# Kernel tuning notes

Hardware: AMD Instinct MI355X
Metric: run time of the kernel (lower is better)

## Reference

```python
import jax, jax.numpy as jnp
import numpy as np

M1 = M2 = M3 = 8  # retained modes per spatial dim


def get_3d_clifford_kernel(w, g):
    # w: (8, O, I, 2m1, 2m2, 2m3); returns (8O, 8I, 2m1, 2m2, 2m3)
    g0, g1, g2 = g[0], g[1], g[2]
    k0 = jnp.concatenate([w[0], w[1] * g0, w[2] * g1, w[3] * g2, -w[4] * g0 * g1, -w[5] * g0 * g2, -w[6] * g1 * g2, -w[7] * g0 * g1 * g2], axis=1)
    k1 = jnp.concatenate([w[1], w[0], -w[4] * g1, -w[5] * g2, w[2] * g1, w[3] * g2, -w[7] * g1 * g2, -w[6] * g1 * g2], axis=1)
    k2 = jnp.concatenate([w[2], w[4] * g0, w[0], -w[6] * g2, -w[1] * g0, w[7] * g0 * g2, w[3] * g2, w[5] * g0 * g2], axis=1)
    k3 = jnp.concatenate([w[3], w[5] * g0, w[6] * g1, w[0], -w[7] * g0 * g1, -w[1] * g0, -w[2] * g1, -w[4] * g0 * g1], axis=1)
    k4 = jnp.concatenate([w[4], w[2], -w[1], g2 * w[7], w[0], -w[6] * g2, w[5] * g2, w[3] * g2], axis=1)
    k5 = jnp.concatenate([w[5], w[3], -w[7] * g1, -w[1], w[6] * g1, w[0], -w[4] * g1, -w[2] * g1], axis=1)
    k6 = jnp.concatenate([w[6], w[7] * g0, w[3], -w[2], -w[5] * g0, w[4] * g0, w[0], w[1] * g0], axis=1)
    k7 = jnp.concatenate([w[7], w[6], -w[5], w[4], w[3], -w[2], w[1], w[0]], axis=1)
    return jnp.concatenate([k0, k1, k2, k3, k4, k5, k6, k7], axis=0)


def setup_inputs() -> dict:
    key = jax.random.key(0)
    k1, k2 = jax.random.split(key)
    B, D, H, W, Cin, Cout = 4, 48, 48, 48, 24, 24
    x = jax.random.normal(k1, (B, D, H, W, Cin, 8), dtype=jnp.float32)
    scale = 1.0 / (Cin * Cout)
    weights = scale * jax.random.uniform(k2, (8, Cout, Cin, 2 * M1, 2 * M2, 2 * M3), dtype=jnp.float32)
    return {"x": x, "weights": weights}


def reference(x, weights):
    B, D, H, W, Cin, _ = x.shape
    Cout = weights.shape[1]
    g = jnp.ones(3, dtype=x.dtype)  # metric (1, 1, 1)
    # complex-dual packing of the 8 blades
    d1 = x[..., 0] + 1j * x[..., 7]
    d2 = x[..., 1] + 1j * x[..., 6]
    d3 = x[..., 2] + 1j * x[..., 5]
    d4 = x[..., 3] + 1j * x[..., 4]
    f1 = jnp.fft.fftn(d1, axes=(1, 2, 3))
    f2 = jnp.fft.fftn(d2, axes=(1, 2, 3))
    f3 = jnp.fft.fftn(d3, axes=(1, 2, 3))
    f4 = jnp.fft.fftn(d4, axes=(1, 2, 3))
    bchw = lambda t: t.transpose(0, 4, 1, 2, 3)
    # (B, 8*Cin, D, H, W) real tensor of blade spectra
    mv_ft = jnp.concatenate([bchw(f1.real), bchw(f2.real), bchw(f3.real), bchw(f4.real),
                             bchw(f4.imag), bchw(f3.imag), bchw(f2.imag), bchw(f1.imag)], axis=1)
    # gather the 8 low/high-frequency octant corners -> (B, 8Cin, 2m1, 2m2, 2m3)
    i1 = jnp.concatenate([jnp.arange(M1), jnp.arange(D - M1, D)])
    i2 = jnp.concatenate([jnp.arange(M2), jnp.arange(H - M2, H)])
    i3 = jnp.concatenate([jnp.arange(M3), jnp.arange(W - M3, W)])
    input_mul = mv_ft[:, :, i1[:, None, None], i2[None, :, None], i3[None, None, :]]
    kernel = get_3d_clifford_kernel(weights, g)  # (8Cout, 8Cin, 2m1, 2m2, 2m3)
    output_mul = jnp.einsum("bixyz,oixyz->boxyz", input_mul, kernel)
    # scatter back to full spectrum
    out_ft = jnp.zeros((B, 8 * Cout, D, H, W), dtype=mv_ft.dtype)
    out_ft = out_ft.at[:, :, i1[:, None, None], i2[None, :, None], i3[None, None, :]].set(output_mul)
    out_ft = out_ft.reshape(B, 8, Cout, D, H, W).transpose(0, 2, 3, 4, 5, 1)  # (B, Cout, D, H, W, 8)
    o1 = out_ft[..., 0] + 1j * out_ft[..., 7]
    o2 = out_ft[..., 1] + 1j * out_ft[..., 6]
    o3 = out_ft[..., 2] + 1j * out_ft[..., 5]
    o4 = out_ft[..., 3] + 1j * out_ft[..., 4]
    g1_ = jnp.fft.ifftn(o1, axes=(2, 3, 4))
    g2_ = jnp.fft.ifftn(o2, axes=(2, 3, 4))
    g3_ = jnp.fft.ifftn(o3, axes=(2, 3, 4))
    g4_ = jnp.fft.ifftn(o4, axes=(2, 3, 4))
    output = jnp.stack([g1_.real, g2_.real, g3_.real, g4_.real,
                        g4_.imag, g3_.imag, g2_.imag, g1_.imag], axis=-1)  # (B, Cout, D, H, W, 8)
    return output.transpose(0, 2, 3, 4, 1, 5)  # (B, D, H, W, Cout, 8)
```

## Files before the change

kernel.cpp:

```cpp
#include <hip/hip_runtime.h>
#include <math.h>


#define C866 0.8660254037844386f

constexpr float FC0[8] = {1.0f, 0.99144486137885f, 0.96592582628907f, 0.92387953251129f,
                          0.86602540378444f, 0.79335334029124f, 0.70710678118655f, 0.60876142900872f};
constexpr float FS0[8] = {0.0f, 0.13052619222005f, 0.25881904510252f, 0.38268343236509f,
                          0.5f, 0.60876142900872f, 0.70710678118655f, 0.79335334029124f};
constexpr float FC1[8] = {0.5f, 0.60876142900872f, 0.70710678118655f, 0.79335334029124f,
                          0.86602540378444f, 0.92387953251129f, 0.96592582628907f, 0.99144486137885f};
constexpr float FS1[8] = {-0.86602540378444f, -0.79335334029124f, -0.70710678118655f, -0.60876142900872f,
                          -0.5f, -0.38268343236509f, -0.25881904510252f, -0.13052619222005f};

__device__ __forceinline__ float2 cmul(float2 a, float2 b) {
  return make_float2(fmaf(a.x, b.x, -(a.y * b.y)), fmaf(a.x, b.y, a.y * b.x));
}
__device__ __forceinline__ void cfma(float2& acc, float2 a, float2 t) {
  acc.x = fmaf(a.x, t.x, acc.x); acc.x = fmaf(-a.y, t.y, acc.x);
  acc.y = fmaf(a.x, t.y, acc.y); acc.y = fmaf(a.y, t.x, acc.y);
}

struct FwdState {
  float2 acc[8], t[8], stp[8];
  float2 R1, R2;
};

__device__ __forceinline__ void fwd_init(FwdState& st, int half) {
#pragma unroll
  for (int r = 0; r < 8; ++r) {
    st.acc[r] = make_float2(0.f, 0.f);
    st.t[r] = make_float2(1.f, 0.f);
    st.stp[r] = make_float2(half ? FC1[r] : FC0[r],
                            half ? -FS1[r] : -FS0[r]);
  }
  st.R1 = half ? make_float2(-0.5f, -C866) : make_float2(1.f, 0.f);
  st.R2 = half ? make_float2(-0.5f,  C866) : make_float2(1.f, 0.f);
}

__device__ __forceinline__ void fwd_stepf(FwdState& st, float2 z0, float2 z1, float2 z2) {
  z1 = cmul(z1, st.R1);
  z2 = cmul(z2, st.R2);
  const float sx = z1.x + z2.x, sy = z1.y + z2.y;
  const float dx = z1.x - z2.x, dy = z1.y - z2.y;
  const float2 y0 = make_float2(z0.x + sx, z0.y + sy);
  const float tx = fmaf(-0.5f, sx, z0.x), ty = fmaf(-0.5f, sy, z0.y);
  const float ex = C866 * dx, ey = C866 * dy;
  const float2 y1 = make_float2(tx + ey, ty - ex);
  const float2 y2 = make_float2(tx - ey, ty + ex);
#pragma unroll
  for (int r = 0; r < 8; ++r) {
    const float2 yy = (r % 3 == 0) ? y0 : ((r % 3 == 1) ? y1 : y2);
    cfma(st.acc[r], yy, st.t[r]);
    st.t[r] = cmul(st.t[r], st.stp[r]);
  }
}

struct InvState {
  float2 zr[16], t[16];
};

__device__ __forceinline__ void inv_init(InvState& st) {
#pragma unroll
  for (int m = 0; m < 16; ++m) st.t[m] = make_float2(1.f, 0.f);
}

__device__ __forceinline__ void inv_stepf(InvState& st, float2& o0, float2& o1, float2& o2) {
  constexpr int JG[16] = {0,1,2,0,1,2,0,1, 1,2,0,1,2,0,1,2};
  float2 u0 = make_float2(0.f, 0.f), u1 = u0, u2 = u0;
#pragma unroll
  for (int m = 0; m < 16; ++m) {
    float2& uu = (JG[m] == 0) ? u0 : ((JG[m] == 1) ? u1 : u2);
    cfma(uu, st.zr[m], st.t[m]);
    const float2 stp = (m < 8) ? make_float2(FC0[m], FS0[m])
                               : make_float2(FC1[m - 8], FS1[m - 8]);
    st.t[m] = cmul(st.t[m], stp);
  }
  const float sx = u1.x + u2.x, sy = u1.y + u2.y;
  const float dx = u1.x - u2.x, dy = u1.y - u2.y;
  o0 = make_float2(u0.x + sx, u0.y + sy);
  const float tx = fmaf(-0.5f, sx, u0.x), ty = fmaf(-0.5f, sy, u0.y);
  const float ex = C866 * dx, ey = C866 * dy;
  o1 = make_float2(tx - ey, ty + ex);
  o2 = make_float2(tx + ey, ty - ex);
}

__global__ __launch_bounds__(192) void k_fwd_w(const float* __restrict__ x,
                                               float2* __restrict__ A) {
  __shared__ __align__(16) float2 xs[48 * 96];
  {
    const float* xp = x + (size_t)blockIdx.x * 9216;
    for (int idx = threadIdx.x; idx < 1152; idx += 192) {
      const int w = idx / 24, ci = idx % 24;
      const float4 u = *(const float4*)(xp + w * 192 + ci * 8);
      const float4 v = *(const float4*)(xp + w * 192 + ci * 8 + 4);
      float4* dst = (float4*)(&xs[w * 96 + ci * 4]);
      dst[0] = make_float4(u.x, v.w, u.y, v.z);
      dst[1] = make_float4(u.z, v.y, u.w, v.x);
    }
  }
  __syncthreads();

  const int q = threadIdx.x % 96, half = threadIdx.x / 96;
  FwdState st;
  fwd_init(st, half);
#pragma unroll 4
  for (int j = 0; j < 16; ++j) {
    const float2 z0 = xs[j * 96 + q];
    const float2 z1 = xs[(j + 16) * 96 + q];
    const float2 z2 = xs[(j + 32) * 96 + q];
    fwd_stepf(st, z0, z1, z2);
  }
  float2* Ap = A + (size_t)blockIdx.x * 1536 + q;
#pragma unroll
  for (int r = 0; r < 8; ++r) Ap[(half * 8 + r) * 96] = st.acc[r];
}

__global__ __launch_bounds__(192) void k_fwd_h(const float2* __restrict__ A,
                                               float2* __restrict__ Bv) {
  const int k3 = blockIdx.x & 15, bd = blockIdx.x >> 4;
  const int q = threadIdx.x % 96, half = threadIdx.x / 96;
  const float2* Ap = A + ((size_t)bd * 768 + k3) * 96 + q;
  FwdState st;
  fwd_init(st, half);
  for (int j = 0; j < 16; ++j) {
    const float2 z0 = Ap[(size_t)j * 1536];
    const float2 z1 = Ap[(size_t)(j + 16) * 1536];
    const float2 z2 = Ap[(size_t)(j + 32) * 1536];
    fwd_stepf(st, z0, z1, z2);
  }
  float2* Bp = Bv + ((size_t)bd * 256 + k3) * 96 + q;
#pragma unroll
  for (int r = 0; r < 8; ++r) Bp[(size_t)(half * 8 + r) * 1536] = st.acc[r];
}

__global__ __launch_bounds__(192) void k_fwd_d(const float2* __restrict__ Bv,
                                               float2* __restrict__ Cv) {
  const int k23 = blockIdx.x & 255, b = blockIdx.x >> 8;
  const int q = threadIdx.x % 96, half = threadIdx.x / 96;
  const float2* Bp = Bv + ((size_t)b * 12288 + k23) * 96 + q;
  FwdState st;
  fwd_init(st, half);
  for (int j = 0; j < 16; ++j) {
    const float2 z0 = Bp[(size_t)j * 24576];
    const float2 z1 = Bp[(size_t)(j + 16) * 24576];
    const float2 z2 = Bp[(size_t)(j + 32) * 24576];
    fwd_stepf(st, z0, z1, z2);
  }
  float2* Cp = Cv + ((size_t)b * 4096 + k23) * 96 + q;
#pragma unroll
  for (int r = 0; r < 8; ++r) Cp[(size_t)(half * 8 + r) * 24576] = st.acc[r];
}

__global__ __launch_bounds__(256) void k_einsum(const float2* __restrict__ Cv,
                                                const float* __restrict__ wgt,
                                                float2* __restrict__ OMz) {
  const int mode = blockIdx.x * 64 + (threadIdx.x & 63);
  const int co = blockIdx.y * 4 + (threadIdx.x >> 6);

  constexpr int WIDX[8][8] = {
      {0, 1, 2, 3, 4, 5, 6, 7}, {1, 0, 4, 5, 2, 3, 7, 6},
      {2, 4, 0, 6, 1, 7, 3, 5}, {3, 5, 6, 0, 7, 1, 2, 4},
      {4, 2, 1, 7, 0, 6, 5, 3}, {5, 3, 7, 1, 6, 0, 4, 2},
      {6, 7, 3, 2, 5, 4, 0, 1}, {7, 6, 5, 4, 3, 2, 1, 0}};
  constexpr int SGN[8][8] = {
      {1, 1, 1, 1, -1, -1, -1, -1}, {1, 1, -1, -1, 1, 1, -1, -1},
      {1, 1, 1, -1, -1, 1, 1, 1},   {1, 1, 1, 1, -1, -1, -1, -1},
      {1, 1, -1, 1, 1, -1, 1, 1},   {1, 1, -1, -1, 1, 1, -1, -1},
      {1, 1, 1, -1, -1, 1, 1, 1},   {1, 1, -1, 1, 1, -1, 1, 1}};

  float acc[8][4];
#pragma unroll
  for (int bo = 0; bo < 8; ++bo)
#pragma unroll
    for (int b = 0; b < 4; ++b) acc[bo][b] = 0.f;

  for (int ci = 0; ci < 24; ++ci) {
    float w8[8];
#pragma unroll
    for (int k = 0; k < 8; ++k)
      w8[k] = wgt[(size_t)((k * 24 + co) * 24 + ci) * 4096 + mode];
#pragma unroll
    for (int b = 0; b < 4; ++b) {
      const float4* cp =
          (const float4*)(Cv + ((size_t)(b * 4096 + mode) * 96 + ci * 4));
      const float4 u = cp[0], v = cp[1];
      const float inv[8] = {u.x, u.z, v.x, v.z, v.w, v.y, u.w, u.y};
#pragma unroll
      for (int bo = 0; bo < 8; ++bo) {
#pragma unroll
        for (int bi = 0; bi < 8; ++bi) {
          const float wv = w8[WIDX[bo][bi]];
          if (SGN[bo][bi] > 0)
            acc[bo][b] = fmaf(wv, inv[bi], acc[bo][b]);
          else
            acc[bo][b] = fmaf(wv, -inv[bi], acc[bo][b]);
        }
      }
    }
  }
#pragma unroll
  for (int b = 0; b < 4; ++b) {
    float2* op = OMz + ((size_t)(b * 4096 + mode) * 96 + co * 4);
#pragma unroll
    for (int c = 0; c < 4; ++c) op[c] = make_float2(acc[c][b], acc[7 - c][b]);
  }
}

__global__ __launch_bounds__(192) void k_inv_d(const float2* __restrict__ OMz,
                                               float2* __restrict__ IS1) {
  const int col = blockIdx.x * 2 + threadIdx.x / 96;
  const int q = threadIdx.x % 96;
  const int k23 = col & 255, b = col >> 8;
  InvState st;
#pragma unroll
  for (int m = 0; m < 16; ++m)
    st.zr[m] = OMz[((size_t)b * 4096 + m * 256 + k23) * 96 + q];
  inv_init(st);
  float2* Op = IS1 + ((size_t)b * 12288 + k23) * 96 + q;
  for (int j = 0; j < 16; ++j) {
    float2 o0, o1, o2;
    inv_stepf(st, o0, o1, o2);
    Op[(size_t)j * 24576] = o0;
    Op[(size_t)(j + 16) * 24576] = o1;
    Op[(size_t)(j + 32) * 24576] = o2;
  }
}

__global__ __launch_bounds__(192) void k_inv_h(const float2* __restrict__ IS1,
                                               float2* __restrict__ IS2) {
  const int col = blockIdx.x * 2 + threadIdx.x / 96;
  const int q = threadIdx.x % 96;
  const int m3 = col & 15, bd = col >> 4;
  InvState st;
#pragma unroll
  for (int m = 0; m < 16; ++m)
    st.zr[m] = IS1[((size_t)bd * 256 + m * 16 + m3) * 96 + q];
  inv_init(st);
  float2* Op = IS2 + ((size_t)bd * 768 + m3) * 96 + q;
  for (int j = 0; j < 16; ++j) {
    float2 o0, o1, o2;
    inv_stepf(st, o0, o1, o2);
    Op[(size_t)j * 1536] = o0;
    Op[(size_t)(j + 16) * 1536] = o1;
    Op[(size_t)(j + 32) * 1536] = o2;
  }
}

__global__ __launch_bounds__(192) void k_inv_w(const float2* __restrict__ IS2,
                                               float* __restrict__ out) {
  const int blk = blockIdx.x * 2 + threadIdx.x / 96;
  const int q = threadIdx.x % 96;
  const int co = q >> 2, c = q & 3;
  const float norm = 1.0f / 110592.0f;
  InvState st;
#pragma unroll
  for (int m = 0; m < 16; ++m) {
    float2 z = IS2[((size_t)blk * 16 + m) * 96 + q];
    st.zr[m] = make_float2(z.x * norm, z.y * norm);
  }
  inv_init(st);
  float* ob = out + (size_t)blk * 9216 + co * 8;
  for (int j = 0; j < 16; ++j) {
    float2 o0, o1, o2;
    inv_stepf(st, o0, o1, o2);
    float* p0 = ob + (size_t)j * 192;
    float* p1 = ob + (size_t)(j + 16) * 192;
    float* p2 = ob + (size_t)(j + 32) * 192;
    p0[c] = o0.x; p0[7 - c] = o0.y;
    p1[c] = o1.x; p1[7 - c] = o1.y;
    p2[c] = o2.x; p2[7 - c] = o2.y;
  }
}

extern "C" void kernel_launch(void* const* d_in, const int* in_sizes, int n_in,
                              void* d_out, int out_size, void* d_ws, size_t ws_size,
                              hipStream_t stream) {
  (void)in_sizes; (void)n_in; (void)out_size; (void)ws_size;
  const float* x = (const float*)d_in[0];
  const float* wgt = (const float*)d_in[1];
  float* out = (float*)d_out;

  char* ob = (char*)d_out;
  float2* A   = (float2*)(ob + 0);
  float2* Bv  = (float2*)(ob + 113246208);
  float2* Cv  = (float2*)(ob + 150994944);
  float2* OMz = (float2*)(ob + 163577856);
  float2* IS1 = (float2*)(ob + 0);
  float2* IS2 = (float2*)d_ws;

  k_fwd_w<<<9216, 192, 0, stream>>>(x, A);
  k_fwd_h<<<3072, 192, 0, stream>>>(A, Bv);
  k_fwd_d<<<1024, 192, 0, stream>>>(Bv, Cv);
  k_einsum<<<dim3(64, 6), 256, 0, stream>>>(Cv, wgt, OMz);
  k_inv_d<<<512, 192, 0, stream>>>(OMz, IS1);
  k_inv_h<<<1536, 192, 0, stream>>>(IS1, IS2);
  k_inv_w<<<4608, 192, 0, stream>>>(IS2, out);
}
```

Baseline: 351.2 us.

## Store FFT intermediates as fp16 and split einsum reduction over Cin halves

Intermediate spectra between the FFT stages (and the input staged in shared memory) are now stored as packed half-precision complex pairs instead of float2. This halves the global and shared memory traffic of these bandwidth-bound passes. Separately, the einsum kernel doubles its block size and splits the Cin loop across two thread groups, combining their partial sums through shared memory to get more parallelism. The fp16 storage reduces accuracy and risks overflow or precision loss against the fp32 reference.

```diff
diff --git a/kernel.cpp b/kernel.cpp
--- a/kernel.cpp
+++ b/kernel.cpp
@@ -12,6 +12,17 @@
                           0.86602540378444f, 0.92387953251129f, 0.96592582628907f, 0.99144486137885f};
 constexpr float FS1[8] = {-0.86602540378444f, -0.79335334029124f, -0.70710678118655f, -0.60876142900872f,
                           -0.5f, -0.38268343236509f, -0.25881904510252f, -0.13052619222005f};
+
+__device__ __forceinline__ uint32_t c2h(float2 z) {
+  union { _Float16 h[2]; uint32_t u; } v;
+  v.h[0] = (_Float16)z.x; v.h[1] = (_Float16)z.y;
+  return v.u;
+}
+__device__ __forceinline__ float2 h2c(uint32_t u) {
+  union { uint32_t u; _Float16 h[2]; } v;
+  v.u = u;
+  return make_float2((float)v.h[0], (float)v.h[1]);
+}
 
 __device__ __forceinline__ float2 cmul(float2 a, float2 b) {
   return make_float2(fmaf(a.x, b.x, -(a.y * b.y)), fmaf(a.x, b.y, a.y * b.x));
@@ -86,17 +97,20 @@
 }
 
 __global__ __launch_bounds__(192) void k_fwd_w(const float* __restrict__ x,
-                                               float2* __restrict__ A) {
-  __shared__ __align__(16) float2 xs[48 * 96];
+                                               uint32_t* __restrict__ A) {
+  __shared__ __align__(16) uint32_t xs[48 * 96];
   {
     const float* xp = x + (size_t)blockIdx.x * 9216;
     for (int idx = threadIdx.x; idx < 1152; idx += 192) {
       const int w = idx / 24, ci = idx % 24;
       const float4 u = *(const float4*)(xp + w * 192 + ci * 8);
       const float4 v = *(const float4*)(xp + w * 192 + ci * 8 + 4);
-      float4* dst = (float4*)(&xs[w * 96 + ci * 4]);
-      dst[0] = make_float4(u.x, v.w, u.y, v.z);
-      dst[1] = make_float4(u.z, v.y, u.w, v.x);
+      uint4 d;
+      d.x = c2h(make_float2(u.x, v.w));
+      d.y = c2h(make_float2(u.y, v.z));
+      d.z = c2h(make_float2(u.z, v.y));
+      d.w = c2h(make_float2(u.w, v.x));
+      *(uint4*)(&xs[w * 96 + ci * 4]) = d;
     }
   }
   __syncthreads();
@@ -106,45 +120,45 @@
   fwd_init(st, half);
 #pragma unroll 4
   for (int j = 0; j < 16; ++j) {
-    const float2 z0 = xs[j * 96 + q];
-    const float2 z1 = xs[(j + 16) * 96 + q];
-    const float2 z2 = xs[(j + 32) * 96 + q];
+    const float2 z0 = h2c(xs[j * 96 + q]);
+    const float2 z1 = h2c(xs[(j + 16) * 96 + q]);
+    const float2 z2 = h2c(xs[(j + 32) * 96 + q]);
     fwd_stepf(st, z0, z1, z2);
   }
-  float2* Ap = A + (size_t)blockIdx.x * 1536 + q;
-#pragma unroll
-  for (int r = 0; r < 8; ++r) Ap[(half * 8 + r) * 96] = st.acc[r];
-}
-
-__global__ __launch_bounds__(192) void k_fwd_h(const float2* __restrict__ A,
-                                               float2* __restrict__ Bv) {
+  uint32_t* Ap = A + (size_t)blockIdx.x * 1536 + q;
+#pragma unroll
+  for (int r = 0; r < 8; ++r) Ap[(half * 8 + r) * 96] = c2h(st.acc[r]);
+}
+
+__global__ __launch_bounds__(192) void k_fwd_h(const uint32_t* __restrict__ A,
+                                               uint32_t* __restrict__ Bv) {
   const int k3 = blockIdx.x & 15, bd = blockIdx.x >> 4;
   const int q = threadIdx.x % 96, half = threadIdx.x / 96;
-  const float2* Ap = A + ((size_t)bd * 768 + k3) * 96 + q;
+  const uint32_t* Ap = A + ((size_t)bd * 768 + k3) * 96 + q;
   FwdState st;
   fwd_init(st, half);
   for (int j = 0; j < 16; ++j) {
-    const float2 z0 = Ap[(size_t)j * 1536];
-    const float2 z1 = Ap[(size_t)(j + 16) * 1536];
-    const float2 z2 = Ap[(size_t)(j + 32) * 1536];
+    const float2 z0 = h2c(Ap[(size_t)j * 1536]);
+    const float2 z1 = h2c(Ap[(size_t)(j + 16) * 1536]);
+    const float2 z2 = h2c(Ap[(size_t)(j + 32) * 1536]);
     fwd_stepf(st, z0, z1, z2);
   }
-  float2* Bp = Bv + ((size_t)bd * 256 + k3) * 96 + q;
-#pragma unroll
-  for (int r = 0; r < 8; ++r) Bp[(size_t)(half * 8 + r) * 1536] = st.acc[r];
-}
-
-__global__ __launch_bounds__(192) void k_fwd_d(const float2* __restrict__ Bv,
+  uint32_t* Bp = Bv + ((size_t)bd * 256 + k3) * 96 + q;
+#pragma unroll
+  for (int r = 0; r < 8; ++r) Bp[(size_t)(half * 8 + r) * 1536] = c2h(st.acc[r]);
+}
+
+__global__ __launch_bounds__(192) void k_fwd_d(const uint32_t* __restrict__ Bv,
                                                float2* __restrict__ Cv) {
   const int k23 = blockIdx.x & 255, b = blockIdx.x >> 8;
   const int q = threadIdx.x % 96, half = threadIdx.x / 96;
-  const float2* Bp = Bv + ((size_t)b * 12288 + k23) * 96 + q;
+  const uint32_t* Bp = Bv + ((size_t)b * 12288 + k23) * 96 + q;
   FwdState st;
   fwd_init(st, half);
   for (int j = 0; j < 16; ++j) {
-    const float2 z0 = Bp[(size_t)j * 24576];
-    const float2 z1 = Bp[(size_t)(j + 16) * 24576];
-    const float2 z2 = Bp[(size_t)(j + 32) * 24576];
+    const float2 z0 = h2c(Bp[(size_t)j * 24576]);
+    const float2 z1 = h2c(Bp[(size_t)(j + 16) * 24576]);
+    const float2 z2 = h2c(Bp[(size_t)(j + 32) * 24576]);
     fwd_stepf(st, z0, z1, z2);
   }
   float2* Cp = Cv + ((size_t)b * 4096 + k23) * 96 + q;
@@ -152,11 +166,16 @@
   for (int r = 0; r < 8; ++r) Cp[(size_t)(half * 8 + r) * 24576] = st.acc[r];
 }
 
-__global__ __launch_bounds__(256) void k_einsum(const float2* __restrict__ Cv,
+__global__ __launch_bounds__(512) void k_einsum(const float2* __restrict__ Cv,
                                                 const float* __restrict__ wgt,
                                                 float2* __restrict__ OMz) {
-  const int mode = blockIdx.x * 64 + (threadIdx.x & 63);
-  const int co = blockIdx.y * 4 + (threadIdx.x >> 6);
+  const int lane = threadIdx.x & 63;
+  const int mode = blockIdx.x * 64 + lane;
+  const int sub = threadIdx.x >> 6;
+  const int col = sub & 3;
+  const int cih = sub >> 2;
+  const int co = blockIdx.y * 4 + col;
+  const int ci0 = cih * 12;
 
   constexpr int WIDX[8][8] = {
       {0, 1, 2, 3, 4, 5, 6, 7}, {1, 0, 4, 5, 2, 3, 7, 6},
@@ -175,7 +194,7 @@
 #pragma unroll
     for (int b = 0; b < 4; ++b) acc[bo][b] = 0.f;
 
-  for (int ci = 0; ci < 24; ++ci) {
+  for (int ci = ci0; ci < ci0 + 12; ++ci) {
     float w8[8];
 #pragma unroll
     for (int k = 0; k < 8; ++k)
@@ -199,16 +218,31 @@
       }
     }
   }
-#pragma unroll
-  for (int b = 0; b < 4; ++b) {
-    float2* op = OMz + ((size_t)(b * 4096 + mode) * 96 + co * 4);
-#pragma unroll
-    for (int c = 0; c < 4; ++c) op[c] = make_float2(acc[c][b], acc[7 - c][b]);
+
+  __shared__ float red[32][4][64];
+  if (cih == 1) {
+#pragma unroll
+    for (int bo = 0; bo < 8; ++bo)
+#pragma unroll
+      for (int b = 0; b < 4; ++b) red[bo * 4 + b][col][lane] = acc[bo][b];
+  }
+  __syncthreads();
+  if (cih == 0) {
+#pragma unroll
+    for (int bo = 0; bo < 8; ++bo)
+#pragma unroll
+      for (int b = 0; b < 4; ++b) acc[bo][b] += red[bo * 4 + b][col][lane];
+#pragma unroll
+    for (int b = 0; b < 4; ++b) {
+      float2* op = OMz + ((size_t)(b * 4096 + mode) * 96 + co * 4);
+#pragma unroll
+      for (int c = 0; c < 4; ++c) op[c] = make_float2(acc[c][b], acc[7 - c][b]);
+    }
   }
 }
 
 __global__ __launch_bounds__(192) void k_inv_d(const float2* __restrict__ OMz,
-                                               float2* __restrict__ IS1) {
+                                               uint32_t* __restrict__ IS1) {
   const int col = blockIdx.x * 2 + threadIdx.x / 96;
   const int q = threadIdx.x % 96;
   const int k23 = col & 255, b = col >> 8;
@@ -217,37 +251,37 @@
   for (int m = 0; m < 16; ++m)
     st.zr[m] = OMz[((size_t)b * 4096 + m * 256 + k23) * 96 + q];
   inv_init(st);
-  float2* Op = IS1 + ((size_t)b * 12288 + k23) * 96 + q;
+  uint32_t* Op = IS1 + ((size_t)b * 12288 + k23) * 96 + q;
   for (int j = 0; j < 16; ++j) {
     float2 o0, o1, o2;
     inv_stepf(st, o0, o1, o2);
-    Op[(size_t)j * 24576] = o0;
-    Op[(size_t)(j + 16) * 24576] = o1;
-    Op[(size_t)(j + 32) * 24576] = o2;
-  }
-}
-
-__global__ __launch_bounds__(192) void k_inv_h(const float2* __restrict__ IS1,
-                                               float2* __restrict__ IS2) {
+    Op[(size_t)j * 24576] = c2h(o0);
+    Op[(size_t)(j + 16) * 24576] = c2h(o1);
+    Op[(size_t)(j + 32) * 24576] = c2h(o2);
+  }
+}
+
+__global__ __launch_bounds__(192) void k_inv_h(const uint32_t* __restrict__ IS1,
+                                               uint32_t* __restrict__ IS2) {
   const int col = blockIdx.x * 2 + threadIdx.x / 96;
   const int q = threadIdx.x % 96;
   const int m3 = col & 15, bd = col >> 4;
   InvState st;
 #pragma unroll
   for (int m = 0; m < 16; ++m)
-    st.zr[m] = IS1[((size_t)bd * 256 + m * 16 + m3) * 96 + q];
+    st.zr[m] = h2c(IS1[((size_t)bd * 256 + m * 16 + m3) * 96 + q]);
   inv_init(st);
-  float2* Op = IS2 + ((size_t)bd * 768 + m3) * 96 + q;
+  uint32_t* Op = IS2 + ((size_t)bd * 768 + m3) * 96 + q;
   for (int j = 0; j < 16; ++j) {
     float2 o0, o1, o2;
     inv_stepf(st, o0, o1, o2);
-    Op[(size_t)j * 1536] = o0;
-    Op[(size_t)(j + 16) * 1536] = o1;
-    Op[(size_t)(j + 32) * 1536] = o2;
-  }
-}
-
-__global__ __launch_bounds__(192) void k_inv_w(const float2* __restrict__ IS2,
+    Op[(size_t)j * 1536] = c2h(o0);
+    Op[(size_t)(j + 16) * 1536] = c2h(o1);
+    Op[(size_t)(j + 32) * 1536] = c2h(o2);
+  }
+}
+
+__global__ __launch_bounds__(192) void k_inv_w(const uint32_t* __restrict__ IS2,
                                                float* __restrict__ out) {
   const int blk = blockIdx.x * 2 + threadIdx.x / 96;
   const int q = threadIdx.x % 96;
@@ -256,7 +290,7 @@
   InvState st;
 #pragma unroll
   for (int m = 0; m < 16; ++m) {
-    float2 z = IS2[((size_t)blk * 16 + m) * 96 + q];
+    float2 z = h2c(IS2[((size_t)blk * 16 + m) * 96 + q]);
     st.zr[m] = make_float2(z.x * norm, z.y * norm);
   }
   inv_init(st);
@@ -282,17 +316,17 @@
   float* out = (float*)d_out;
 
   char* ob = (char*)d_out;
-  float2* A   = (float2*)(ob + 0);
-  float2* Bv  = (float2*)(ob + 113246208);
-  float2* Cv  = (float2*)(ob + 150994944);
-  float2* OMz = (float2*)(ob + 163577856);
-  float2* IS1 = (float2*)(ob + 0);
-  float2* IS2 = (float2*)d_ws;
+  uint32_t* A   = (uint32_t*)(ob + 0);
+  uint32_t* Bv  = (uint32_t*)(ob + 56623104);
+  float2*   Cv  = (float2*)(ob + 75497472);
+  float2*   OMz = (float2*)(ob + 88080384);
+  uint32_t* IS1 = (uint32_t*)(ob + 0);
+  uint32_t* IS2 = (uint32_t*)d_ws;
 
   k_fwd_w<<<9216, 192, 0, stream>>>(x, A);
   k_fwd_h<<<3072, 192, 0, stream>>>(A, Bv);
   k_fwd_d<<<1024, 192, 0, stream>>>(Bv, Cv);
-  k_einsum<<<dim3(64, 6), 256, 0, stream>>>(Cv, wgt, OMz);
+  k_einsum<<<dim3(64, 6), 512, 0, stream>>>(Cv, wgt, OMz);
   k_inv_d<<<512, 192, 0, stream>>>(OMz, IS1);
   k_inv_h<<<1536, 192, 0, stream>>>(IS1, IS2);
   k_inv_w<<<4608, 192, 0, stream>>>(IS2, out);
```

New measurement: 361.1 us. 1.03x slower.
